# Kernel tuning notes

Hardware: AMD Instinct MI355X
Metric: run time of the kernel (lower is better)

The kernel has to match this reference:

```python
import jax, jax.numpy as jnp
import numpy as np

N0, D, H, E0 = 50000, 128, 128, 800000
N1, E1, A, B, C = 20000, 320000, 100000, 64, 10


def _gcn(x, row, col, ew, n, W, b):
    # GCNConv: out = D^-1/2 (A + I) D^-1/2 (x W) + b, with edge weights
    xw = x @ W
    sl = jnp.arange(n)
    r = jnp.concatenate([row, sl])
    c = jnp.concatenate([col, sl])
    w = jnp.concatenate([ew, jnp.ones((n,), ew.dtype)])
    deg = jax.ops.segment_sum(w, c, num_segments=n)
    dinv = jax.lax.rsqrt(jnp.maximum(deg, 1e-12))
    norm = dinv[r] * w * dinv[c]
    return jax.ops.segment_sum(norm[:, None] * xw[r], c, num_segments=n) + b


def _block(x, row, col, ew, n, W1, b1, W2, b2, Wl, bl):
    # Block with num_inner_layers=2, jumping_knowledge='cat'
    x1 = jax.nn.relu(_gcn(x, row, col, ew, n, W1, b1))
    x2 = jax.nn.relu(_gcn(x1, row, col, ew, n, W2, b2))
    return jnp.concatenate([x1, x2], axis=1) @ Wl + bl


def _seg_max(x, idx, n):
    m = jax.ops.segment_max(x, idx, num_segments=n)
    return jnp.where(jnp.isfinite(m), m, 0.0)  # empty segments -> 0 like scatter_max default


def _lin_init(k, i, o):
    s = 1.0 / np.sqrt(i)
    return jax.random.uniform(k, (i, o), jnp.float32, -s, s)


def setup_inputs() -> dict:
    key = jax.random.key(0)
    ks = jax.random.split(key, 20)
    x = jax.random.normal(ks[0], (N0, D), jnp.float32)
    edge_index0 = jax.random.randint(ks[1], (2, E0), 0, N0)
    edge_weight0 = jax.random.uniform(ks[2], (E0,), jnp.float32)
    batch0 = jnp.sort(jax.random.randint(ks[3], (N0,), 0, B))
    cover_row = jax.random.randint(ks[4], (A,), 0, N0)
    cover_col = jnp.concatenate([jnp.arange(N1), jax.random.randint(ks[5], (A - N1,), 0, N1)])
    edge_index1 = jax.random.randint(ks[6], (2, E1), 0, N1)
    edge_weight1 = jax.random.uniform(ks[7], (E1,), jnp.float32)
    batch1 = jnp.sort(jax.random.randint(ks[8], (N1,), 0, B))
    params = dict(
        w_in1=_lin_init(ks[9], D, H), b_in1=jnp.zeros((H,), jnp.float32),
        w_in2=_lin_init(ks[10], H, H), b_in2=jnp.zeros((H,), jnp.float32),
        w_in_lin=_lin_init(ks[11], 2 * H, H), b_in_lin=jnp.zeros((H,), jnp.float32),
        w_b1=_lin_init(ks[12], 2 * H, H), b_b1=jnp.zeros((H,), jnp.float32),
        w_b2=_lin_init(ks[13], H, H), b_b2=jnp.zeros((H,), jnp.float32),
        w_b_lin=_lin_init(ks[14], 2 * H, H), b_b_lin=jnp.zeros((H,), jnp.float32),
        bn_gamma=jnp.ones((4 * H,), jnp.float32), bn_beta=jnp.zeros((4 * H,), jnp.float32),
        w_l1=_lin_init(ks[15], 4 * H, H), b_l1=jnp.zeros((H,), jnp.float32),
        w_l2=_lin_init(ks[16], H, C), b_l2=jnp.zeros((C,), jnp.float32),
    )
    return dict(x=x, edge_index0=edge_index0, edge_weight0=edge_weight0, batch0=batch0,
                cover_row=cover_row, cover_col=cover_col, edge_index1=edge_index1,
                edge_weight1=edge_weight1, batch1=batch1, **params)


def reference(x, edge_index0, edge_weight0, batch0, cover_row, cover_col,
              edge_index1, edge_weight1, batch1,
              w_in1, b_in1, w_in2, b_in2, w_in_lin, b_in_lin,
              w_b1, b_b1, w_b2, b_b2, w_b_lin, b_b_lin,
              bn_gamma, bn_beta, w_l1, b_l1, w_l2, b_l2):
    r0, c0 = edge_index0[0], edge_index0[1]
    h = jax.nn.relu(_block(x, r0, c0, edge_weight0, N0, w_in1, b_in1, w_in2, b_in2, w_in_lin, b_in_lin))
    xs = [jax.ops.segment_sum(h, batch0, num_segments=B), _seg_max(h, batch0, B)]
    # cover_pool_node: add + max over k-plex cover assignments
    hg = h[cover_row]
    h2 = jnp.concatenate([jax.ops.segment_sum(hg, cover_col, num_segments=N1),
                          _seg_max(hg, cover_col, N1)], axis=1)
    r1, c1 = edge_index1[0], edge_index1[1]
    h2 = jax.nn.relu(_block(h2, r1, c1, edge_weight1, N1, w_b1, b_b1, w_b2, b_b2, w_b_lin, b_b_lin))
    xs.append(jax.ops.segment_sum(h2, batch1, num_segments=B))
    xs.append(_seg_max(h2, batch1, B))
    z = jnp.concatenate(xs, axis=1)  # [B, 4H]
    # BatchNorm1d in eval mode: running stats (mean=0, var=1), eps=1e-5
    z = z * (bn_gamma * jax.lax.rsqrt(jnp.asarray(1.0 + 1e-5, z.dtype))) + bn_beta
    z = jax.nn.relu(z @ w_l1 + b_l1)
    logits = z @ w_l2 + b_l2  # dropout skipped (eval mode)
    return jax.nn.softmax(logits, axis=-1)
```

## Files before the change

kernel.cpp:

```cpp
#include <hip/hip_runtime.h>
#include <cmath>

#define HF 128

namespace {

typedef __attribute__((ext_vector_type(8))) short short8;
typedef __attribute__((ext_vector_type(4))) float f32x4;

inline int cdiv(int a, int b) { return (a + b - 1) / b; }

__device__ inline unsigned short f2bf(float x) {
    unsigned u = __float_as_uint(x);
    return (unsigned short)((u + 0x7fffu + ((u >> 16) & 1u)) >> 16);
}
__device__ inline float bf2f(unsigned short u) {
    return __uint_as_float((unsigned)u << 16);
}
__device__ inline float bflo(unsigned v) { return __uint_as_float(v << 16); }
__device__ inline float bfhi(unsigned v) { return __uint_as_float(v & 0xffff0000u); }

#define FIXS 4194304.0f
#define FIXINV 2.384185791015625e-07f
#define SUMMASK ((1ULL << 40) - 1)

template <int K, bool AF32>
__device__ __forceinline__ void gemm_dev(int bid, const void* __restrict__ A1v, int lda1,
                                         const void* __restrict__ A2v, int lda2,
                                         const unsigned short* __restrict__ wpk,
                                         const float* __restrict__ bias, int relu,
                                         unsigned short* __restrict__ out, int N) {
    const int t = threadIdx.x;
    const int wv = t >> 6, lane = t & 63;
    const int l15 = lane & 15, lhi = lane >> 4;
    const int rbase = bid * 128 + wv * 32;

    f32x4 acc[2][8];
#pragma unroll
    for (int i = 0; i < 2; ++i)
#pragma unroll
        for (int g = 0; g < 8; ++g) acc[i][g] = {0.f, 0.f, 0.f, 0.f};

    int r[2];
#pragma unroll
    for (int ri = 0; ri < 2; ++ri) {
        int rr = rbase + ri * 16 + l15;
        r[ri] = (rr < N) ? rr : (N - 1);
    }

    for (int kc = 0; kc < K / 32; ++kc) {
        int kb = kc * 32 + lhi * 8;
        short8 a[2];
#pragma unroll
        for (int ri = 0; ri < 2; ++ri) {
            if (AF32) {
                const float* A = (const float*)A1v;
                const float* p = A + (size_t)r[ri] * lda1 + kb;
                float4 f0 = *reinterpret_cast<const float4*>(p);
                float4 f1 = *reinterpret_cast<const float4*>(p + 4);
                a[ri][0] = (short)f2bf(f0.x); a[ri][1] = (short)f2bf(f0.y);
                a[ri][2] = (short)f2bf(f0.z); a[ri][3] = (short)f2bf(f0.w);
                a[ri][4] = (short)f2bf(f1.x); a[ri][5] = (short)f2bf(f1.y);
                a[ri][6] = (short)f2bf(f1.z); a[ri][7] = (short)f2bf(f1.w);
            } else {
                const unsigned short* base;
                int kk, ld;
                if (K == 256 && kb >= 128) { base = (const unsigned short*)A2v; kk = kb - 128; ld = lda2; }
                else                       { base = (const unsigned short*)A1v; kk = kb;       ld = lda1; }
                a[ri] = *reinterpret_cast<const short8*>(base + (size_t)r[ri] * ld + kk);
            }
        }
        const unsigned short* wb = wpk + (size_t)(kc * 8) * 512 + lane * 8;
#pragma unroll
        for (int g = 0; g < 8; ++g) {
            short8 b = *reinterpret_cast<const short8*>(wb + (size_t)g * 512);
            acc[0][g] = __builtin_amdgcn_mfma_f32_16x16x32_bf16(a[0], b, acc[0][g], 0, 0, 0);
            acc[1][g] = __builtin_amdgcn_mfma_f32_16x16x32_bf16(a[1], b, acc[1][g], 0, 0, 0);
        }
    }

#pragma unroll
    for (int ri = 0; ri < 2; ++ri) {
#pragma unroll
        for (int g = 0; g < 8; ++g) {
            int col = l15 + g * 16;
            float bb = bias ? bias[col] : 0.f;
#pragma unroll
            for (int e = 0; e < 4; ++e) {
                int rr = rbase + ri * 16 + lhi * 4 + e;
                if (rr < N) {
                    float v = acc[ri][g][e] + bb;
                    if (relu) v = fmaxf(v, 0.f);
                    out[(size_t)rr * 128 + col] = f2bf(v);
                }
            }
        }
    }
}

template <int K, bool AF32>
__global__ void k_mfma_gemm(const void* __restrict__ A1v, int lda1,
                            const void* __restrict__ A2v, int lda2,
                            const unsigned short* __restrict__ wpk,
                            const float* __restrict__ bias, int relu,
                            unsigned short* __restrict__ out, int N) {
    gemm_dev<K, AF32>(blockIdx.x, A1v, lda1, A2v, lda2, wpk, bias, relu, out, N);
}

__global__ void k_prep0(const float* __restrict__ w0, const float* __restrict__ w1,
                        const float* __restrict__ w2, const float* __restrict__ w3,
                        const float* __restrict__ w4, const float* __restrict__ w5,
                        unsigned short* __restrict__ wpk,
                        const int* __restrict__ b0, int n0, const int* __restrict__ b1,
                        int n1, int B, int* __restrict__ bst0, int* __restrict__ bst1) {
    int b = blockIdx.x, t = threadIdx.x;
    if (b < 576) {
        int idx = b * 256 + t;
        const float* src; int local;
        if      (idx < 16384)  { src = w0; local = idx; }
        else if (idx < 32768)  { src = w1; local = idx - 16384; }
        else if (idx < 65536)  { src = w2; local = idx - 32768; }
        else if (idx < 98304)  { src = w3; local = idx - 65536; }
        else if (idx < 114688) { src = w4; local = idx - 98304; }
        else                   { src = w5; local = idx - 114688; }
        int e = local & 7, lane = (local >> 3) & 63, g = (local >> 9) & 7, kc = local >> 12;
        int colw = (lane & 15) + 16 * g;
        int k = kc * 32 + ((lane >> 4) << 3) + e;
        wpk[idx] = f2bf(src[k * 128 + colw]);
        return;
    }
    {
        int idx = t;
        if (idx < 2 * (B + 1)) {
            int which = idx > B;
            int bb = which ? idx - (B + 1) : idx;
            const int* arr = which ? b1 : b0;
            int lo = 0, hi = which ? n1 : n0;
            while (lo < hi) {
                int mid = (lo + hi) >> 1;
                if (arr[mid] < bb) lo = mid + 1; else hi = mid;
            }
            (which ? bst1 : bst0)[bb] = lo;
        }
    }
}

__global__ void k_prep1(const float* __restrict__ x, const unsigned short* __restrict__ wpk,
                        unsigned short* __restrict__ xw, int N0gemm, int nbG,
                        const int* __restrict__ col0, const float* __restrict__ ew0,
                        unsigned long long* __restrict__ dc0, unsigned* __restrict__ rank0,
                        int E0, int nb0,
                        const int* __restrict__ col1, const float* __restrict__ ew1,
                        unsigned long long* __restrict__ dc1, unsigned* __restrict__ rank1,
                        int E1, int nb1,
                        const int* __restrict__ ccol, int* __restrict__ ccnt,
                        unsigned* __restrict__ rankc, int A) {
    int b = blockIdx.x, t = threadIdx.x;
    if (b < nbG) {
        gemm_dev<128, true>(b, x, 128, nullptr, 0, wpk, nullptr, 0, xw, N0gemm);
        return;
    }
    b -= nbG;
    if (b < nb0) {
        int e = b * 256 + t;
        if (e < E0) {
            unsigned long long v = (1ULL << 40) | (unsigned long long)(ew0[e] * FIXS + 0.5f);
            unsigned long long old = atomicAdd(&dc0[col0[e]], v);
            rank0[e] = (unsigned)(old >> 40);
        }
        return;
    }
    b -= nb0;
    if (b < nb1) {
        int e = b * 256 + t;
        if (e < E1) {
            unsigned long long v = (1ULL << 40) | (unsigned long long)(ew1[e] * FIXS + 0.5f);
            unsigned long long old = atomicAdd(&dc1[col1[e]], v);
            rank1[e] = (unsigned)(old >> 40);
        }
        return;
    }
    b -= nb1;
    {
        int e = b * 256 + t;
        if (e < A) rankc[e] = (unsigned)atomicAdd(&ccnt[ccol[e]], 1);
    }
}

__device__ inline void scan256(int* s, int v, int gid, int n, int* __restrict__ excl,
                               int* __restrict__ partial, int pb) {
    s[threadIdx.x] = v;
    __syncthreads();
    for (int off = 1; off < 256; off <<= 1) {
        int t = (threadIdx.x >= off) ? s[threadIdx.x - off] : 0;
        __syncthreads();
        s[threadIdx.x] += t;
        __syncthreads();
    }
    if (gid < n) excl[gid] = s[threadIdx.x] - v;
    if (threadIdx.x == 255) partial[pb] = s[255];
}

__global__ void k_scan_dinv(const unsigned long long* __restrict__ dc0, int* __restrict__ rp0,
                            int* __restrict__ part0, int n0, int nbs0,
                            const unsigned long long* __restrict__ dc1, int* __restrict__ rp1,
                            int* __restrict__ part1, int n1, int nbs1,
                            const int* __restrict__ ccnt, int* __restrict__ crp,
                            int* __restrict__ cpart, int nc, int nbsc,
                            float* __restrict__ dinv0, float* __restrict__ dinv1,
                            int nbd0, int nbd1) {
    __shared__ int s[256];
    int b = blockIdx.x, t = threadIdx.x;
    if (b < nbs0) {
        int gid = b * 256 + t;
        int v = (gid < n0) ? (int)(dc0[gid] >> 40) : 0;
        scan256(s, v, gid, n0, rp0, part0, b);
        return;
    }
    b -= nbs0;
    if (b < nbs1) {
        int gid = b * 256 + t;
        int v = (gid < n1) ? (int)(dc1[gid] >> 40) : 0;
        scan256(s, v, gid, n1, rp1, part1, b);
        return;
    }
    b -= nbs1;
    if (b < nbsc) {
        int gid = b * 256 + t;
        int v = (gid < nc) ? ccnt[gid] : 0;
        scan256(s, v, gid, nc, crp, cpart, b);
        return;
    }
    b -= nbsc;
    if (b < nbd0) {
        int i = b * 256 + t;
        if (i < n0) dinv0[i] = rsqrtf(1.0f + (float)(dc0[i] & SUMMASK) * FIXINV);
        return;
    }
    b -= nbd0;
    {
        int i = b * 256 + t;
        if (i < n1) dinv1[i] = rsqrtf(1.0f + (float)(dc1[i] & SUMMASK) * FIXINV);
    }
}

__global__ void k_scan2x3(int* __restrict__ p0, int nb0, int* __restrict__ p1, int nb1,
                          int* __restrict__ p2, int nb2) {
    __shared__ int s[256];
    int* p; int nb;
    if (blockIdx.x == 0)      { p = p0; nb = nb0; }
    else if (blockIdx.x == 1) { p = p1; nb = nb1; }
    else                      { p = p2; nb = nb2; }
    int v = (threadIdx.x < nb) ? p[threadIdx.x] : 0;
    s[threadIdx.x] = v;
    __syncthreads();
    for (int off = 1; off < 256; off <<= 1) {
        int t = (threadIdx.x >= off) ? s[threadIdx.x - off] : 0;
        __syncthreads();
        s[threadIdx.x] += t;
        __syncthreads();
    }
    if (threadIdx.x < nb) p[threadIdx.x] = s[threadIdx.x] - v;
}

__global__ void k_scan3x3(int* __restrict__ rp0, const int* __restrict__ part0,
                          int n0, int tot0, int nb0,
                          int* __restrict__ rp1, const int* __restrict__ part1,
                          int n1, int tot1, int nb1,
                          int* __restrict__ crp, const int* __restrict__ cpart,
                          int nc, int totc) {
    int b = blockIdx.x, t = threadIdx.x;
    if (b < nb0) {
        int gid = b * 256 + t;
        if (gid < n0) rp0[gid] += part0[b];
        if (gid == 0) rp0[n0] = tot0;
        return;
    }
    b -= nb0;
    if (b < nb1) {
        int gid = b * 256 + t;
        if (gid < n1) rp1[gid] += part1[b];
        if (gid == 0) rp1[n1] = tot1;
        return;
    }
    b -= nb1;
    {
        int gid = b * 256 + t;
        if (gid < nc) crp[gid] += cpart[b];
        if (gid == 0) crp[nc] = totc;
    }
}

#define EPB 2048
__global__ void k_fillx3(const int* __restrict__ row0, const int* __restrict__ col0,
                         const float* __restrict__ ew0, const unsigned* __restrict__ rank0,
                         const float* __restrict__ dinv0, const int* __restrict__ rp0,
                         int2* __restrict__ ed0, int E0, int N0n, int g0b,
                         const int* __restrict__ row1, const int* __restrict__ col1,
                         const float* __restrict__ ew1, const unsigned* __restrict__ rank1,
                         const float* __restrict__ dinv1, const int* __restrict__ rp1,
                         int2* __restrict__ ed1, int E1, int N1n, int g1b,
                         const int* __restrict__ crow, const int* __restrict__ ccol,
                         const unsigned* __restrict__ rankc, const int* __restrict__ crp,
                         int* __restrict__ csrcs, int A) {
    int b = blockIdx.x, t = threadIdx.x;
    if (b < g0b) {
        int xcd = b & 7, chunk = b >> 3;
        int lo = (int)((long long)N0n * xcd >> 3), hi = (int)((long long)N0n * (xcd + 1) >> 3);
        int base = chunk * EPB;
#pragma unroll
        for (int i = 0; i < EPB; i += 256) {
            int e = base + i + t;
            if (e < E0) {
                int c = col0[e];
                if (c >= lo && c < hi) {
                    int r = row0[e];
                    ed0[rp0[c] + rank0[e]] =
                        make_int2(r, __float_as_int(ew0[e] * dinv0[r] * dinv0[c]));
                }
            }
        }
        return;
    }
    b -= g0b;
    if (b < g1b) {
        int xcd = b & 7, chunk = b >> 3;
        int lo = (int)((long long)N1n * xcd >> 3), hi = (int)((long long)N1n * (xcd + 1) >> 3);
        int base = chunk * EPB;
#pragma unroll
        for (int i = 0; i < EPB; i += 256) {
            int e = base + i + t;
            if (e < E1) {
                int c = col1[e];
                if (c >= lo && c < hi) {
                    int r = row1[e];
                    ed1[rp1[c] + rank1[e]] =
                        make_int2(r, __float_as_int(ew1[e] * dinv1[r] * dinv1[c]));
                }
            }
        }
        return;
    }
    b -= g1b;
    {
        int xcd = b & 7, chunk = b >> 3;
        int lo = (int)((long long)N1n * xcd >> 3), hi = (int)((long long)N1n * (xcd + 1) >> 3);
        int base = chunk * EPB;
#pragma unroll
        for (int i = 0; i < EPB; i += 256) {
            int e = base + i + t;
            if (e < A) {
                int c = ccol[e];
                if (c >= lo && c < hi) csrcs[crp[c] + rankc[e]] = crow[e];
            }
        }
    }
}

__global__ void k_gcn_gather(const unsigned* __restrict__ xw, const int* __restrict__ rowptr,
                             const int2* __restrict__ ed, const float* __restrict__ dinv,
                             const float* __restrict__ bias, unsigned* __restrict__ out, int n) {
    int wid = (blockIdx.x * 256 + threadIdx.x) >> 6;
    if (wid >= n) return;
    int lane = threadIdx.x & 63;
    int s = rowptr[wid], e = rowptr[wid + 1];
    float d = dinv[wid];
    unsigned v = xw[(size_t)wid * 64 + lane];
    float ax = bflo(v) * d * d, ay = bfhi(v) * d * d;
    float bx = 0.f, by = 0.f, cx = 0.f, cy = 0.f, dx = 0.f, dy = 0.f;
    int i = s;
    if ((i & 1) && i < e) {
        int2 e0 = ed[i];
        unsigned v0 = xw[(size_t)e0.x * 64 + lane];
        float c0 = __int_as_float(e0.y);
        ax += c0 * bflo(v0); ay += c0 * bfhi(v0);
        ++i;
    }
    for (; i + 4 <= e; i += 4) {
        int4 q0 = *reinterpret_cast<const int4*>(ed + i);
        int4 q1 = *reinterpret_cast<const int4*>(ed + i + 2);
        unsigned v0 = xw[(size_t)q0.x * 64 + lane];
        unsigned v1 = xw[(size_t)q0.z * 64 + lane];
        unsigned v2 = xw[(size_t)q1.x * 64 + lane];
        unsigned v3 = xw[(size_t)q1.z * 64 + lane];
        float c0 = __int_as_float(q0.y), c1 = __int_as_float(q0.w);
        float c2 = __int_as_float(q1.y), c3 = __int_as_float(q1.w);
        ax += c0 * bflo(v0); ay += c0 * bfhi(v0);
        bx += c1 * bflo(v1); by += c1 * bfhi(v1);
        cx += c2 * bflo(v2); cy += c2 * bfhi(v2);
        dx += c3 * bflo(v3); dy += c3 * bfhi(v3);
    }
    for (; i < e; ++i) {
        int2 e0 = ed[i];
        unsigned v0 = xw[(size_t)e0.x * 64 + lane];
        float c0 = __int_as_float(e0.y);
        ax += c0 * bflo(v0); ay += c0 * bfhi(v0);
    }
    ax += bx + cx + dx;
    ay += by + cy + dy;
    float2 bb = *reinterpret_cast<const float2*>(bias + lane * 2);
    ax = fmaxf(ax + bb.x, 0.f);
    ay = fmaxf(ay + bb.y, 0.f);
    out[(size_t)wid * 64 + lane] = (unsigned)f2bf(ax) | ((unsigned)f2bf(ay) << 16);
}

__global__ void k_pool_cover(const unsigned short* __restrict__ h, const int* __restrict__ bst,
                             float* __restrict__ psum, float* __restrict__ pmax, int nsplit,
                             int nbpool, const unsigned* __restrict__ h32,
                             const int* __restrict__ crp, const int* __restrict__ csrcs,
                             unsigned* __restrict__ h2, int n1) {
    int t = threadIdx.x;
    if ((int)blockIdx.x < nbpool) {
        int blk = blockIdx.x;
        int b = blk / nsplit, sub = (blk % nsplit) * 2 + (t >> 7);
        int col = t & 127;
        int r0 = bst[b], r1 = bst[b + 1];
        float sum = 0.f, mx = 0.f;
        for (int r = r0 + sub; r < r1; r += 2 * nsplit) {
            float v = bf2f(h[(size_t)r * HF + col]);
            sum += v;
            mx = fmaxf(mx, v);
        }
        atomicAdd(&psum[b * HF + col], sum);
        atomicMax(reinterpret_cast<int*>(&pmax[b * HF + col]), __float_as_int(mx));
        return;
    }
    int wid = (((int)blockIdx.x - nbpool) * 256 + t) >> 6;
    if (wid >= n1) return;
    int lane = t & 63;
    int s = crp[wid], e = crp[wid + 1];
    float sx = 0.f, sy = 0.f, mx = 0.f, my = 0.f;
    for (int i = s; i < e; ++i) {
        unsigned v = h32[(size_t)csrcs[i] * 64 + lane];
        float vx = bflo(v), vy = bfhi(v);
        sx += vx; sy += vy;
        mx = fmaxf(mx, vx); my = fmaxf(my, vy);
    }
    h2[(size_t)wid * 128 + lane]      = (unsigned)f2bf(sx) | ((unsigned)f2bf(sy) << 16);
    h2[(size_t)wid * 128 + 64 + lane] = (unsigned)f2bf(mx) | ((unsigned)f2bf(my) << 16);
}

__global__ void k_pool256(const unsigned short* __restrict__ h, const int* __restrict__ bst,
                          float* __restrict__ psum, float* __restrict__ pmax, int nsplit) {
    int t = threadIdx.x;
    int blk = blockIdx.x;
    int b = blk / nsplit, sub = (blk % nsplit) * 2 + (t >> 7);
    int col = t & 127;
    int r0 = bst[b], r1 = bst[b + 1];
    float sum = 0.f, mx = 0.f;
    for (int r = r0 + sub; r < r1; r += 2 * nsplit) {
        float v = bf2f(h[(size_t)r * HF + col]);
        sum += v;
        mx = fmaxf(mx, v);
    }
    atomicAdd(&psum[b * HF + col], sum);
    atomicMax(reinterpret_cast<int*>(&pmax[b * HF + col]), __float_as_int(mx));
}

__global__ void k_head(const float* __restrict__ p0s, const float* __restrict__ p0m,
                       const float* __restrict__ p1s, const float* __restrict__ p1m,
                       const float* __restrict__ gamma, const float* __restrict__ beta,
                       const float* __restrict__ w1, const float* __restrict__ b1,
                       const float* __restrict__ w2, const float* __restrict__ b2,
                       float* __restrict__ out) {
    __shared__ float z[512];
    __shared__ float z1[128];
    __shared__ float lg[10];
    int b = blockIdx.x, t = threadIdx.x;
    const float s = rsqrtf(1.0f + 1e-5f);
    z[t]       = p0s[b * 128 + t] * (gamma[t] * s)       + beta[t];
    z[128 + t] = p0m[b * 128 + t] * (gamma[128 + t] * s) + beta[128 + t];
    z[256 + t] = p1s[b * 128 + t] * (gamma[256 + t] * s) + beta[256 + t];
    z[384 + t] = p1m[b * 128 + t] * (gamma[384 + t] * s) + beta[384 + t];
    __syncthreads();
    float acc = b1[t];
    for (int k = 0; k < 512; ++k) acc += z[k] * w1[k * 128 + t];
    z1[t] = fmaxf(acc, 0.f);
    __syncthreads();
    if (t < 10) {
        float a2 = b2[t];
        for (int k = 0; k < 128; ++k) a2 += z1[k] * w2[k * 10 + t];
        lg[t] = a2;
    }
    __syncthreads();
    if (t == 0) {
        float m = lg[0];
        for (int c = 1; c < 10; ++c) m = fmaxf(m, lg[c]);
        float e[10], ssum = 0.f;
        for (int c = 0; c < 10; ++c) { e[c] = expf(lg[c] - m); ssum += e[c]; }
        for (int c = 0; c < 10; ++c) out[b * 10 + c] = e[c] / ssum;
    }
}

}

extern "C" void kernel_launch(void* const* d_in, const int* in_sizes, int n_in,
                              void* d_out, int out_size, void* d_ws, size_t ws_size,
                              hipStream_t stream) {
    const float* x      = (const float*)d_in[0];
    const int*   ei0    = (const int*)d_in[1];
    const float* ew0    = (const float*)d_in[2];
    const int*   batch0 = (const int*)d_in[3];
    const int*   crow   = (const int*)d_in[4];
    const int*   ccol   = (const int*)d_in[5];
    const int*   ei1    = (const int*)d_in[6];
    const float* ew1    = (const float*)d_in[7];
    const int*   batch1 = (const int*)d_in[8];
    const float* w_in1  = (const float*)d_in[9];
    const float* b_in1  = (const float*)d_in[10];
    const float* w_in2  = (const float*)d_in[11];
    const float* b_in2  = (const float*)d_in[12];
    const float* w_inl  = (const float*)d_in[13];
    const float* b_inl  = (const float*)d_in[14];
    const float* w_b1   = (const float*)d_in[15];
    const float* b_b1   = (const float*)d_in[16];
    const float* w_b2   = (const float*)d_in[17];
    const float* b_b2   = (const float*)d_in[18];
    const float* w_bl   = (const float*)d_in[19];
    const float* b_bl   = (const float*)d_in[20];
    const float* gamma  = (const float*)d_in[21];
    const float* beta   = (const float*)d_in[22];
    const float* w_l1   = (const float*)d_in[23];
    const float* b_l1   = (const float*)d_in[24];
    const float* w_l2   = (const float*)d_in[25];
    const float* b_l2   = (const float*)d_in[26];

    const int N0 = in_sizes[0] / 128;
    const int E0 = in_sizes[2];
    const int A  = in_sizes[4];
    const int E1 = in_sizes[7];
    const int N1 = in_sizes[8];
    const int B  = out_size / 10;

    const int* row0 = ei0;
    const int* col0 = ei0 + E0;
    const int* row1 = ei1;
    const int* col1 = ei1 + E1;

    char* wsp = (char*)d_ws;
    size_t off = 0;
    auto alloc = [&](size_t bytes) -> char* {
        char* p = wsp + off;
        off += (bytes + 255) & ~(size_t)255;
        return p;
    };
    unsigned long long* dc0 = (unsigned long long*)alloc((size_t)N0 * 8);
    unsigned long long* dc1 = (unsigned long long*)alloc((size_t)N1 * 8);
    int*   ccnt  = (int*)alloc((size_t)N1 * 4);
    float* p0s   = (float*)alloc((size_t)B * HF * 4 * 4);
    float* p0m   = p0s + (size_t)B * HF;
    float* p1s   = p0m + (size_t)B * HF;
    float* p1m   = p1s + (size_t)B * HF;
    size_t zero_bytes = off;

    unsigned* xw  = (unsigned*)alloc((size_t)N0 * 64 * 4);
    unsigned* x1  = (unsigned*)alloc((size_t)N0 * 64 * 4);
    unsigned* x2  = (unsigned*)alloc((size_t)N0 * 64 * 4);
    unsigned* h   = (unsigned*)alloc((size_t)N0 * 64 * 4);
    unsigned* h2  = (unsigned*)alloc((size_t)N1 * 128 * 4);
    unsigned short* wpk = (unsigned short*)alloc(147456 * 2);
    float* dinv0 = (float*)alloc((size_t)N0 * 4);
    float* dinv1 = (float*)alloc((size_t)N1 * 4);
    int*   rp0   = (int*)alloc(((size_t)N0 + 1) * 4);
    int*   rp1   = (int*)alloc(((size_t)N1 + 1) * 4);
    int*   crp   = (int*)alloc(((size_t)N1 + 1) * 4);
    int*   part0 = (int*)alloc(256 * 4);
    int*   part1 = (int*)alloc(256 * 4);
    int*   cpart = (int*)alloc(256 * 4);
    int2*  ed0   = (int2*)alloc((size_t)E0 * 8);
    int2*  ed1   = (int2*)alloc((size_t)E1 * 8);
    int*   csrcs = (int*)alloc((size_t)A * 4);
    unsigned* rank0 = (unsigned*)alloc((size_t)E0 * 4);
    unsigned* rank1 = (unsigned*)alloc((size_t)E1 * 4);
    unsigned* rankc = (unsigned*)alloc((size_t)A * 4);
    int*   bst0  = (int*)alloc((size_t)(B + 1) * 4);
    int*   bst1  = (int*)alloc((size_t)(B + 1) * 4);
    (void)ws_size; (void)n_in;

    const int NSPLIT = 16;
    const int nbG  = cdiv(N0, 128);
    const int nbE0 = cdiv(E0, 256), nbE1 = cdiv(E1, 256), nbC = cdiv(A, 256);
    const int nbs0 = cdiv(N0, 256), nbs1 = cdiv(N1, 256), nbsc = cdiv(N1, 256);
    const int g0b = cdiv(E0, EPB) * 8, g1b = cdiv(E1, EPB) * 8, gcb = cdiv(A, EPB) * 8;

    hipMemsetAsync(dc0, 0, zero_bytes, stream);

    k_prep0<<<577, 256, 0, stream>>>(w_in1, w_in2, w_inl, w_b1, w_b2, w_bl, wpk,
                                     batch0, N0, batch1, N1, B, bst0, bst1);

    k_prep1<<<nbG + nbE0 + nbE1 + nbC, 256, 0, stream>>>(
        x, wpk, (unsigned short*)xw, N0, nbG,
        col0, ew0, dc0, rank0, E0, nbE0,
        col1, ew1, dc1, rank1, E1, nbE1,
        ccol, ccnt, rankc, A);

    k_scan_dinv<<<nbs0 + nbs1 + nbsc + nbs0 + nbs1, 256, 0, stream>>>(
        dc0, rp0, part0, N0, nbs0, dc1, rp1, part1, N1, nbs1,
        ccnt, crp, cpart, N1, nbsc, dinv0, dinv1, nbs0, nbs1);

    k_scan2x3<<<3, 256, 0, stream>>>(part0, nbs0, part1, nbs1, cpart, nbsc);

    k_scan3x3<<<nbs0 + nbs1 + nbsc, 256, 0, stream>>>(
        rp0, part0, N0, E0, nbs0, rp1, part1, N1, E1, nbs1, crp, cpart, N1, A);

    k_fillx3<<<g0b + g1b + gcb, 256, 0, stream>>>(
        row0, col0, ew0, rank0, dinv0, rp0, ed0, E0, N0, g0b,
        row1, col1, ew1, rank1, dinv1, rp1, ed1, E1, N1, g1b,
        crow, ccol, rankc, crp, csrcs, A);

    k_gcn_gather<<<cdiv(N0, 4), 256, 0, stream>>>(xw, rp0, ed0, dinv0, b_in1, x1, N0);
    k_mfma_gemm<128, false><<<cdiv(N0, 128), 256, 0, stream>>>(
        x1, 128, nullptr, 0, wpk + 16384, nullptr, 0, (unsigned short*)xw, N0);
    k_gcn_gather<<<cdiv(N0, 4), 256, 0, stream>>>(xw, rp0, ed0, dinv0, b_in2, x2, N0);
    k_mfma_gemm<256, false><<<cdiv(N0, 128), 256, 0, stream>>>(
        x1, 128, x2, 128, wpk + 32768, b_inl, 1, (unsigned short*)h, N0);

    k_pool_cover<<<B * NSPLIT + cdiv(N1, 4), 256, 0, stream>>>(
        (const unsigned short*)h, bst0, p0s, p0m, NSPLIT, B * NSPLIT,
        h, crp, csrcs, h2, N1);

    k_mfma_gemm<256, false><<<cdiv(N1, 128), 256, 0, stream>>>(
        h2, 256, (const unsigned short*)h2 + 128, 256, wpk + 65536, nullptr, 0,
        (unsigned short*)xw, N1);
    k_gcn_gather<<<cdiv(N1, 4), 256, 0, stream>>>(xw, rp1, ed1, dinv1, b_b1, x1, N1);
    k_mfma_gemm<128, false><<<cdiv(N1, 128), 256, 0, stream>>>(
        x1, 128, nullptr, 0, wpk + 98304, nullptr, 0, (unsigned short*)xw, N1);
    k_gcn_gather<<<cdiv(N1, 4), 256, 0, stream>>>(xw, rp1, ed1, dinv1, b_b2, x2, N1);
    k_mfma_gemm<256, false><<<cdiv(N1, 128), 256, 0, stream>>>(
        x1, 128, x2, 128, wpk + 114688, b_bl, 1, (unsigned short*)h, N1);

    k_pool256<<<B * NSPLIT, 256, 0, stream>>>((const unsigned short*)h, bst1, p1s, p1m, NSPLIT);

    k_head<<<B, 128, 0, stream>>>(p0s, p0m, p1s, p1m, gamma, beta, w_l1, b_l1, w_l2, b_l2,
                                  (float*)d_out);
}
```

Baseline: 381.1 us.

## Shard XW into column planes for gathers and overlap graph-1 preprocessing with block-0 work

GEMMs that feed GCN aggregation now write XW as four 32-column planes. The gather kernel gives each node a 16-lane quarter-wave that works on one plane, which is meant to shrink the gather working set per pass and improve L2 locality for random row reads. The graph-1 histogram, scans and CSR fill are pulled off the critical path and fused as extra blocks into the block-0 gather and GEMM launches, so they overlap with that work. This adds more kernel launches for the graph-0 scan chain, and the gather is less unrolled (two edges per iteration instead of four).

```diff
diff --git a/kernel.cpp b/kernel.cpp
--- a/kernel.cpp
+++ b/kernel.cpp
@@ -2,6 +2,7 @@
 #include <cmath>
 
 #define HF 128
+#define EPB 2048
 
 namespace {
 
@@ -24,7 +25,7 @@
 #define FIXINV 2.384185791015625e-07f
 #define SUMMASK ((1ULL << 40) - 1)
 
-template <int K, bool AF32>
+template <int K, bool AF32, bool PLANES>
 __device__ __forceinline__ void gemm_dev(int bid, const void* __restrict__ A1v, int lda1,
                                          const void* __restrict__ A2v, int lda2,
                                          const unsigned short* __restrict__ wpk,
@@ -91,20 +92,110 @@
                 if (rr < N) {
                     float v = acc[ri][g][e] + bb;
                     if (relu) v = fmaxf(v, 0.f);
-                    out[(size_t)rr * 128 + col] = f2bf(v);
+                    if (PLANES)
+                        out[(size_t)(col >> 5) * ((size_t)N * 32) + (size_t)rr * 32 + (col & 31)] = f2bf(v);
+                    else
+                        out[(size_t)rr * 128 + col] = f2bf(v);
                 }
             }
         }
     }
 }
 
-template <int K, bool AF32>
+template <int K, bool AF32, bool PLANES>
 __global__ void k_mfma_gemm(const void* __restrict__ A1v, int lda1,
                             const void* __restrict__ A2v, int lda2,
                             const unsigned short* __restrict__ wpk,
                             const float* __restrict__ bias, int relu,
                             unsigned short* __restrict__ out, int N) {
-    gemm_dev<K, AF32>(blockIdx.x, A1v, lda1, A2v, lda2, wpk, bias, relu, out, N);
+    gemm_dev<K, AF32, PLANES>(blockIdx.x, A1v, lda1, A2v, lda2, wpk, bias, relu, out, N);
+}
+
+__device__ __forceinline__ void hist_dev(int e, int E, const int* __restrict__ col,
+                                         const float* __restrict__ ew,
+                                         unsigned long long* __restrict__ dc,
+                                         unsigned* __restrict__ rank) {
+    if (e < E) {
+        unsigned long long v = (1ULL << 40) | (unsigned long long)(ew[e] * FIXS + 0.5f);
+        unsigned long long old = atomicAdd(&dc[col[e]], v);
+        rank[e] = (unsigned)(old >> 40);
+    }
+}
+
+__device__ inline void scan256(int* s, int v, int gid, int n, int* __restrict__ excl,
+                               int* __restrict__ partial, int pb) {
+    s[threadIdx.x] = v;
+    __syncthreads();
+    for (int off = 1; off < 256; off <<= 1) {
+        int t = (threadIdx.x >= off) ? s[threadIdx.x - off] : 0;
+        __syncthreads();
+        s[threadIdx.x] += t;
+        __syncthreads();
+    }
+    if (gid < n) excl[gid] = s[threadIdx.x] - v;
+    if (threadIdx.x == 255) partial[pb] = s[255];
+}
+
+__device__ __forceinline__ void fill_dev(int b, int t, const int* __restrict__ row,
+                                         const int* __restrict__ col, const float* __restrict__ ew,
+                                         const unsigned* __restrict__ rank,
+                                         const float* __restrict__ dinv, const int* __restrict__ rp,
+                                         int2* __restrict__ ed, int E, int Nn) {
+    int xcd = b & 7, chunk = b >> 3;
+    int lo = (int)((long long)Nn * xcd >> 3), hi = (int)((long long)Nn * (xcd + 1) >> 3);
+    int base = chunk * EPB;
+#pragma unroll
+    for (int i = 0; i < EPB; i += 256) {
+        int e = base + i + t;
+        if (e < E) {
+            int c = col[e];
+            if (c >= lo && c < hi) {
+                int r = row[e];
+                ed[rp[c] + rank[e]] = make_int2(r, __float_as_int(ew[e] * dinv[r] * dinv[c]));
+            }
+        }
+    }
+}
+
+__device__ __forceinline__ void gather_dev(int b, const unsigned* __restrict__ xwp, int n,
+                                           const int* __restrict__ rp, const int2* __restrict__ ed,
+                                           const float* __restrict__ dinv,
+                                           const float* __restrict__ bias,
+                                           unsigned* __restrict__ out) {
+    int t = threadIdx.x;
+    int shard = b & 3;
+    int lane = t & 63, wv = t >> 6;
+    int dl = lane >> 4, l16 = lane & 15;
+    int wid = (b >> 2) * 16 + wv * 4 + dl;
+    if (wid >= n) return;
+    const unsigned* plane = xwp + (size_t)shard * ((size_t)n * 16);
+    int s = rp[wid], e = rp[wid + 1];
+    float d = dinv[wid];
+    unsigned v = plane[(size_t)wid * 16 + l16];
+    float ax = bflo(v) * d * d, ay = bfhi(v) * d * d, bx = 0.f, by = 0.f;
+    int i = s;
+    for (; i + 2 <= e; i += 2) {
+        unsigned long long p0 = __builtin_nontemporal_load((const unsigned long long*)(ed + i));
+        unsigned long long p1 = __builtin_nontemporal_load((const unsigned long long*)(ed + i + 1));
+        unsigned v0 = plane[(size_t)(unsigned)(p0 & 0xffffffffu) * 16 + l16];
+        unsigned v1 = plane[(size_t)(unsigned)(p1 & 0xffffffffu) * 16 + l16];
+        float c0 = __uint_as_float((unsigned)(p0 >> 32));
+        float c1 = __uint_as_float((unsigned)(p1 >> 32));
+        ax += c0 * bflo(v0); ay += c0 * bfhi(v0);
+        bx += c1 * bflo(v1); by += c1 * bfhi(v1);
+    }
+    if (i < e) {
+        int2 e0 = ed[i];
+        unsigned v0 = plane[(size_t)e0.x * 16 + l16];
+        float c0 = __int_as_float(e0.y);
+        ax += c0 * bflo(v0); ay += c0 * bfhi(v0);
+    }
+    ax += bx; ay += by;
+    float2 bb = *reinterpret_cast<const float2*>(bias + shard * 32 + l16 * 2);
+    ax = fmaxf(ax + bb.x, 0.f);
+    ay = fmaxf(ay + bb.y, 0.f);
+    unsigned o = (unsigned)f2bf(ax) | ((unsigned)f2bf(ay) << 16);
+    __builtin_nontemporal_store(o, out + (size_t)wid * 64 + shard * 16 + l16);
 }
 
 __global__ void k_prep0(const float* __restrict__ w0, const float* __restrict__ w1,
@@ -129,19 +220,17 @@
         wpk[idx] = f2bf(src[k * 128 + colw]);
         return;
     }
-    {
-        int idx = t;
-        if (idx < 2 * (B + 1)) {
-            int which = idx > B;
-            int bb = which ? idx - (B + 1) : idx;
-            const int* arr = which ? b1 : b0;
-            int lo = 0, hi = which ? n1 : n0;
-            while (lo < hi) {
-                int mid = (lo + hi) >> 1;
-                if (arr[mid] < bb) lo = mid + 1; else hi = mid;
-            }
-            (which ? bst1 : bst0)[bb] = lo;
+    int idx = t;
+    if (idx < 2 * (B + 1)) {
+        int which = idx > B;
+        int bb = which ? idx - (B + 1) : idx;
+        const int* arr = which ? b1 : b0;
+        int lo = 0, hi = which ? n1 : n0;
+        while (lo < hi) {
+            int mid = (lo + hi) >> 1;
+            if (arr[mid] < bb) lo = mid + 1; else hi = mid;
         }
+        (which ? bst1 : bst0)[bb] = lo;
     }
 }
 
@@ -149,46 +238,28 @@
                         unsigned short* __restrict__ xw, int N0gemm, int nbG,
                         const int* __restrict__ col0, const float* __restrict__ ew0,
                         unsigned long long* __restrict__ dc0, unsigned* __restrict__ rank0,
-                        int E0, int nb0,
-                        const int* __restrict__ col1, const float* __restrict__ ew1,
-                        unsigned long long* __restrict__ dc1, unsigned* __restrict__ rank1,
-                        int E1, int nb1,
-                        const int* __restrict__ ccol, int* __restrict__ ccnt,
-                        unsigned* __restrict__ rankc, int A) {
-    int b = blockIdx.x, t = threadIdx.x;
+                        int E0) {
+    int b = blockIdx.x;
     if (b < nbG) {
-        gemm_dev<128, true>(b, x, 128, nullptr, 0, wpk, nullptr, 0, xw, N0gemm);
+        gemm_dev<128, true, true>(b, x, 128, nullptr, 0, wpk, nullptr, 0, xw, N0gemm);
         return;
     }
     b -= nbG;
-    if (b < nb0) {
-        int e = b * 256 + t;
-        if (e < E0) {
-            unsigned long long v = (1ULL << 40) | (unsigned long long)(ew0[e] * FIXS + 0.5f);
-            unsigned long long old = atomicAdd(&dc0[col0[e]], v);
-            rank0[e] = (unsigned)(old >> 40);
-        }
-        return;
-    }
-    b -= nb0;
-    if (b < nb1) {
-        int e = b * 256 + t;
-        if (e < E1) {
-            unsigned long long v = (1ULL << 40) | (unsigned long long)(ew1[e] * FIXS + 0.5f);
-            unsigned long long old = atomicAdd(&dc1[col1[e]], v);
-            rank1[e] = (unsigned)(old >> 40);
-        }
-        return;
-    }
-    b -= nb1;
-    {
-        int e = b * 256 + t;
-        if (e < A) rankc[e] = (unsigned)atomicAdd(&ccnt[ccol[e]], 1);
-    }
-}
-
-__device__ inline void scan256(int* s, int v, int gid, int n, int* __restrict__ excl,
-                               int* __restrict__ partial, int pb) {
+    hist_dev(b * 256 + (int)threadIdx.x, E0, col0, ew0, dc0, rank0);
+}
+
+__global__ void k_scanA(const unsigned long long* __restrict__ dc0, int* __restrict__ rp0,
+                        int* __restrict__ part0, float* __restrict__ dinv0, int n0) {
+    __shared__ int s[256];
+    int gid = blockIdx.x * 256 + threadIdx.x;
+    int v = (gid < n0) ? (int)(dc0[gid] >> 40) : 0;
+    scan256(s, v, gid, n0, rp0, part0, blockIdx.x);
+    if (gid < n0) dinv0[gid] = rsqrtf(1.0f + (float)(dc0[gid] & SUMMASK) * FIXINV);
+}
+
+__global__ void k_scan2a(int* __restrict__ p0, int nb0) {
+    __shared__ int s[256];
+    int v = (threadIdx.x < nb0) ? p0[threadIdx.x] : 0;
     s[threadIdx.x] = v;
     __syncthreads();
     for (int off = 1; off < 256; off <<= 1) {
@@ -197,60 +268,73 @@
         s[threadIdx.x] += t;
         __syncthreads();
     }
-    if (gid < n) excl[gid] = s[threadIdx.x] - v;
-    if (threadIdx.x == 255) partial[pb] = s[255];
-}
-
-__global__ void k_scan_dinv(const unsigned long long* __restrict__ dc0, int* __restrict__ rp0,
-                            int* __restrict__ part0, int n0, int nbs0,
+    if (threadIdx.x < nb0) p0[threadIdx.x] = s[threadIdx.x] - v;
+}
+
+__global__ void k_scan3a(int* __restrict__ rp0, const int* __restrict__ part0, int n0, int tot) {
+    int gid = blockIdx.x * 256 + threadIdx.x;
+    if (gid < n0) rp0[gid] += part0[blockIdx.x];
+    if (gid == 0) rp0[n0] = tot;
+}
+
+__global__ void k_fill0(const int* __restrict__ row0, const int* __restrict__ col0,
+                        const float* __restrict__ ew0, const unsigned* __restrict__ rank0,
+                        const float* __restrict__ dinv0, const int* __restrict__ rp0,
+                        int2* __restrict__ ed0, int E0, int N0n) {
+    fill_dev(blockIdx.x, threadIdx.x, row0, col0, ew0, rank0, dinv0, rp0, ed0, E0, N0n);
+}
+
+__global__ void k_gather_hist(const unsigned* __restrict__ xwp, int n,
+                              const int* __restrict__ rp, const int2* __restrict__ ed,
+                              const float* __restrict__ dinv, const float* __restrict__ bias,
+                              unsigned* __restrict__ out, int G,
+                              const int* __restrict__ col1, const float* __restrict__ ew1,
+                              unsigned long long* __restrict__ dc1, unsigned* __restrict__ rank1,
+                              int E1, int nb1,
+                              const int* __restrict__ ccol, int* __restrict__ ccnt,
+                              unsigned* __restrict__ rankc, int A) {
+    int b = blockIdx.x;
+    if (b < G) { gather_dev(b, xwp, n, rp, ed, dinv, bias, out); return; }
+    b -= G;
+    int t = threadIdx.x;
+    if (b < nb1) { hist_dev(b * 256 + t, E1, col1, ew1, dc1, rank1); return; }
+    b -= nb1;
+    int e = b * 256 + t;
+    if (e < A) rankc[e] = (unsigned)atomicAdd(&ccnt[ccol[e]], 1);
+}
+
+__global__ void k_gemm_scan(const void* __restrict__ A1v, const unsigned short* __restrict__ wpk,
+                            unsigned short* __restrict__ out, int N, int nbG,
                             const unsigned long long* __restrict__ dc1, int* __restrict__ rp1,
-                            int* __restrict__ part1, int n1, int nbs1,
+                            int* __restrict__ part1, float* __restrict__ dinv1, int n1, int nbs1,
                             const int* __restrict__ ccnt, int* __restrict__ crp,
-                            int* __restrict__ cpart, int nc, int nbsc,
-                            float* __restrict__ dinv0, float* __restrict__ dinv1,
-                            int nbd0, int nbd1) {
+                            int* __restrict__ cpart, int nc) {
     __shared__ int s[256];
-    int b = blockIdx.x, t = threadIdx.x;
-    if (b < nbs0) {
-        int gid = b * 256 + t;
-        int v = (gid < n0) ? (int)(dc0[gid] >> 40) : 0;
-        scan256(s, v, gid, n0, rp0, part0, b);
+    int b = blockIdx.x;
+    if (b < nbG) {
+        gemm_dev<128, false, true>(b, A1v, 128, nullptr, 0, wpk, nullptr, 0, out, N);
         return;
     }
-    b -= nbs0;
+    b -= nbG;
     if (b < nbs1) {
-        int gid = b * 256 + t;
+        int gid = b * 256 + threadIdx.x;
         int v = (gid < n1) ? (int)(dc1[gid] >> 40) : 0;
         scan256(s, v, gid, n1, rp1, part1, b);
+        if (gid < n1) dinv1[gid] = rsqrtf(1.0f + (float)(dc1[gid] & SUMMASK) * FIXINV);
         return;
     }
     b -= nbs1;
-    if (b < nbsc) {
-        int gid = b * 256 + t;
+    {
+        int gid = b * 256 + threadIdx.x;
         int v = (gid < nc) ? ccnt[gid] : 0;
         scan256(s, v, gid, nc, crp, cpart, b);
-        return;
-    }
-    b -= nbsc;
-    if (b < nbd0) {
-        int i = b * 256 + t;
-        if (i < n0) dinv0[i] = rsqrtf(1.0f + (float)(dc0[i] & SUMMASK) * FIXINV);
-        return;
-    }
-    b -= nbd0;
-    {
-        int i = b * 256 + t;
-        if (i < n1) dinv1[i] = rsqrtf(1.0f + (float)(dc1[i] & SUMMASK) * FIXINV);
-    }
-}
-
-__global__ void k_scan2x3(int* __restrict__ p0, int nb0, int* __restrict__ p1, int nb1,
-                          int* __restrict__ p2, int nb2) {
+    }
+}
+
+__global__ void k_scan2b(int* __restrict__ p1, int nb1, int* __restrict__ p2, int nb2) {
     __shared__ int s[256];
-    int* p; int nb;
-    if (blockIdx.x == 0)      { p = p0; nb = nb0; }
-    else if (blockIdx.x == 1) { p = p1; nb = nb1; }
-    else                      { p = p2; nb = nb2; }
+    int* p = (blockIdx.x == 0) ? p1 : p2;
+    int nb = (blockIdx.x == 0) ? nb1 : nb2;
     int v = (threadIdx.x < nb) ? p[threadIdx.x] : 0;
     s[threadIdx.x] = v;
     __syncthreads();
@@ -263,20 +347,10 @@
     if (threadIdx.x < nb) p[threadIdx.x] = s[threadIdx.x] - v;
 }
 
-__global__ void k_scan3x3(int* __restrict__ rp0, const int* __restrict__ part0,
-                          int n0, int tot0, int nb0,
-                          int* __restrict__ rp1, const int* __restrict__ part1,
-                          int n1, int tot1, int nb1,
-                          int* __restrict__ crp, const int* __restrict__ cpart,
-                          int nc, int totc) {
+__global__ void k_scan3b(int* __restrict__ rp1, const int* __restrict__ part1, int n1, int tot1,
+                         int nb1, int* __restrict__ crp, const int* __restrict__ cpart,
+                         int nc, int totc) {
     int b = blockIdx.x, t = threadIdx.x;
-    if (b < nb0) {
-        int gid = b * 256 + t;
-        if (gid < n0) rp0[gid] += part0[b];
-        if (gid == 0) rp0[n0] = tot0;
-        return;
-    }
-    b -= nb0;
     if (b < nb1) {
         int gid = b * 256 + t;
         if (gid < n1) rp1[gid] += part1[b];
@@ -284,63 +358,26 @@
         return;
     }
     b -= nb1;
-    {
-        int gid = b * 256 + t;
-        if (gid < nc) crp[gid] += cpart[b];
-        if (gid == 0) crp[nc] = totc;
-    }
-}
-
-#define EPB 2048
-__global__ void k_fillx3(const int* __restrict__ row0, const int* __restrict__ col0,
-                         const float* __restrict__ ew0, const unsigned* __restrict__ rank0,
-                         const float* __restrict__ dinv0, const int* __restrict__ rp0,
-                         int2* __restrict__ ed0, int E0, int N0n, int g0b,
-                         const int* __restrict__ row1, const int* __restrict__ col1,
-                         const float* __restrict__ ew1, const unsigned* __restrict__ rank1,
-                         const float* __restrict__ dinv1, const int* __restrict__ rp1,
-                         int2* __restrict__ ed1, int E1, int N1n, int g1b,
-                         const int* __restrict__ crow, const int* __restrict__ ccol,
-                         const unsigned* __restrict__ rankc, const int* __restrict__ crp,
-                         int* __restrict__ csrcs, int A) {
+    int gid = b * 256 + t;
+    if (gid < nc) crp[gid] += cpart[b];
+    if (gid == 0) crp[nc] = totc;
+}
+
+__global__ void k_gather_fill(const unsigned* __restrict__ xwp, int n,
+                              const int* __restrict__ rp, const int2* __restrict__ ed,
+                              const float* __restrict__ dinv, const float* __restrict__ bias,
+                              unsigned* __restrict__ out, int G,
+                              const int* __restrict__ row1, const int* __restrict__ col1,
+                              const float* __restrict__ ew1, const unsigned* __restrict__ rank1,
+                              const float* __restrict__ dinv1, const int* __restrict__ rp1,
+                              int2* __restrict__ ed1, int E1, int N1n, int g1b,
+                              const int* __restrict__ crow, const int* __restrict__ ccol,
+                              const unsigned* __restrict__ rankc, const int* __restrict__ crp,
+                              int* __restrict__ csrcs, int A) {
     int b = blockIdx.x, t = threadIdx.x;
-    if (b < g0b) {
-        int xcd = b & 7, chunk = b >> 3;
-        int lo = (int)((long long)N0n * xcd >> 3), hi = (int)((long long)N0n * (xcd + 1) >> 3);
-        int base = chunk * EPB;
-#pragma unroll
-        for (int i = 0; i < EPB; i += 256) {
-            int e = base + i + t;
-            if (e < E0) {
-                int c = col0[e];
-                if (c >= lo && c < hi) {
-                    int r = row0[e];
-                    ed0[rp0[c] + rank0[e]] =
-                        make_int2(r, __float_as_int(ew0[e] * dinv0[r] * dinv0[c]));
-                }
-            }
-        }
-        return;
-    }
-    b -= g0b;
-    if (b < g1b) {
-        int xcd = b & 7, chunk = b >> 3;
-        int lo = (int)((long long)N1n * xcd >> 3), hi = (int)((long long)N1n * (xcd + 1) >> 3);
-        int base = chunk * EPB;
-#pragma unroll
-        for (int i = 0; i < EPB; i += 256) {
-            int e = base + i + t;
-            if (e < E1) {
-                int c = col1[e];
-                if (c >= lo && c < hi) {
-                    int r = row1[e];
-                    ed1[rp1[c] + rank1[e]] =
-                        make_int2(r, __float_as_int(ew1[e] * dinv1[r] * dinv1[c]));
-                }
-            }
-        }
-        return;
-    }
+    if (b < G) { gather_dev(b, xwp, n, rp, ed, dinv, bias, out); return; }
+    b -= G;
+    if (b < g1b) { fill_dev(b, t, row1, col1, ew1, rank1, dinv1, rp1, ed1, E1, N1n); return; }
     b -= g1b;
     {
         int xcd = b & 7, chunk = b >> 3;
@@ -357,51 +394,10 @@
     }
 }
 
-__global__ void k_gcn_gather(const unsigned* __restrict__ xw, const int* __restrict__ rowptr,
-                             const int2* __restrict__ ed, const float* __restrict__ dinv,
-                             const float* __restrict__ bias, unsigned* __restrict__ out, int n) {
-    int wid = (blockIdx.x * 256 + threadIdx.x) >> 6;
-    if (wid >= n) return;
-    int lane = threadIdx.x & 63;
-    int s = rowptr[wid], e = rowptr[wid + 1];
-    float d = dinv[wid];
-    unsigned v = xw[(size_t)wid * 64 + lane];
-    float ax = bflo(v) * d * d, ay = bfhi(v) * d * d;
-    float bx = 0.f, by = 0.f, cx = 0.f, cy = 0.f, dx = 0.f, dy = 0.f;
-    int i = s;
-    if ((i & 1) && i < e) {
-        int2 e0 = ed[i];
-        unsigned v0 = xw[(size_t)e0.x * 64 + lane];
-        float c0 = __int_as_float(e0.y);
-        ax += c0 * bflo(v0); ay += c0 * bfhi(v0);
-        ++i;
-    }
-    for (; i + 4 <= e; i += 4) {
-        int4 q0 = *reinterpret_cast<const int4*>(ed + i);
-        int4 q1 = *reinterpret_cast<const int4*>(ed + i + 2);
-        unsigned v0 = xw[(size_t)q0.x * 64 + lane];
-        unsigned v1 = xw[(size_t)q0.z * 64 + lane];
-        unsigned v2 = xw[(size_t)q1.x * 64 + lane];
-        unsigned v3 = xw[(size_t)q1.z * 64 + lane];
-        float c0 = __int_as_float(q0.y), c1 = __int_as_float(q0.w);
-        float c2 = __int_as_float(q1.y), c3 = __int_as_float(q1.w);
-        ax += c0 * bflo(v0); ay += c0 * bfhi(v0);
-        bx += c1 * bflo(v1); by += c1 * bfhi(v1);
-        cx += c2 * bflo(v2); cy += c2 * bfhi(v2);
-        dx += c3 * bflo(v3); dy += c3 * bfhi(v3);
-    }
-    for (; i < e; ++i) {
-        int2 e0 = ed[i];
-        unsigned v0 = xw[(size_t)e0.x * 64 + lane];
-        float c0 = __int_as_float(e0.y);
-        ax += c0 * bflo(v0); ay += c0 * bfhi(v0);
-    }
-    ax += bx + cx + dx;
-    ay += by + cy + dy;
-    float2 bb = *reinterpret_cast<const float2*>(bias + lane * 2);
-    ax = fmaxf(ax + bb.x, 0.f);
-    ay = fmaxf(ay + bb.y, 0.f);
-    out[(size_t)wid * 64 + lane] = (unsigned)f2bf(ax) | ((unsigned)f2bf(ay) << 16);
+__global__ void k_gather(const unsigned* __restrict__ xwp, int n, const int* __restrict__ rp,
+                         const int2* __restrict__ ed, const float* __restrict__ dinv,
+                         const float* __restrict__ bias, unsigned* __restrict__ out) {
+    gather_dev(blockIdx.x, xwp, n, rp, ed, dinv, bias, out);
 }
 
 __global__ void k_pool_cover(const unsigned short* __restrict__ h, const int* __restrict__ bst,
@@ -578,56 +574,59 @@
     (void)ws_size; (void)n_in;
 
     const int NSPLIT = 16;
-    const int nbG  = cdiv(N0, 128);
+    const int nbG0 = cdiv(N0, 128), nbG1 = cdiv(N1, 128);
     const int nbE0 = cdiv(E0, 256), nbE1 = cdiv(E1, 256), nbC = cdiv(A, 256);
     const int nbs0 = cdiv(N0, 256), nbs1 = cdiv(N1, 256), nbsc = cdiv(N1, 256);
-    const int g0b = cdiv(E0, EPB) * 8, g1b = cdiv(E1, EPB) * 8, gcb = cdiv(A, EPB) * 8;
+    const int g0f = cdiv(E0, EPB) * 8, g1f = cdiv(E1, EPB) * 8, gcf = cdiv(A, EPB) * 8;
+    const int G0 = cdiv(N0, 16) * 4, G1 = cdiv(N1, 16) * 4;
 
     hipMemsetAsync(dc0, 0, zero_bytes, stream);
 
     k_prep0<<<577, 256, 0, stream>>>(w_in1, w_in2, w_inl, w_b1, w_b2, w_bl, wpk,
                                      batch0, N0, batch1, N1, B, bst0, bst1);
 
-    k_prep1<<<nbG + nbE0 + nbE1 + nbC, 256, 0, stream>>>(
-        x, wpk, (unsigned short*)xw, N0, nbG,
-        col0, ew0, dc0, rank0, E0, nbE0,
-        col1, ew1, dc1, rank1, E1, nbE1,
-        ccol, ccnt, rankc, A);
-
-    k_scan_dinv<<<nbs0 + nbs1 + nbsc + nbs0 + nbs1, 256, 0, stream>>>(
-        dc0, rp0, part0, N0, nbs0, dc1, rp1, part1, N1, nbs1,
-        ccnt, crp, cpart, N1, nbsc, dinv0, dinv1, nbs0, nbs1);
-
-    k_scan2x3<<<3, 256, 0, stream>>>(part0, nbs0, part1, nbs1, cpart, nbsc);
-
-    k_scan3x3<<<nbs0 + nbs1 + nbsc, 256, 0, stream>>>(
-        rp0, part0, N0, E0, nbs0, rp1, part1, N1, E1, nbs1, crp, cpart, N1, A);
-
-    k_fillx3<<<g0b + g1b + gcb, 256, 0, stream>>>(
-        row0, col0, ew0, rank0, dinv0, rp0, ed0, E0, N0, g0b,
-        row1, col1, ew1, rank1, dinv1, rp1, ed1, E1, N1, g1b,
+    k_prep1<<<nbG0 + nbE0, 256, 0, stream>>>(x, wpk, (unsigned short*)xw, N0, nbG0,
+                                             col0, ew0, dc0, rank0, E0);
+
+    k_scanA<<<nbs0, 256, 0, stream>>>(dc0, rp0, part0, dinv0, N0);
+    k_scan2a<<<1, 256, 0, stream>>>(part0, nbs0);
+    k_scan3a<<<nbs0, 256, 0, stream>>>(rp0, part0, N0, E0);
+    k_fill0<<<g0f, 256, 0, stream>>>(row0, col0, ew0, rank0, dinv0, rp0, ed0, E0, N0);
+
+    k_gather_hist<<<G0 + nbE1 + nbC, 256, 0, stream>>>(
+        xw, N0, rp0, ed0, dinv0, b_in1, x1, G0,
+        col1, ew1, dc1, rank1, E1, nbE1, ccol, ccnt, rankc, A);
+
+    k_gemm_scan<<<nbG0 + nbs1 + nbsc, 256, 0, stream>>>(
+        x1, wpk + 16384, (unsigned short*)xw, N0, nbG0,
+        dc1, rp1, part1, dinv1, N1, nbs1, ccnt, crp, cpart, N1);
+
+    k_scan2b<<<2, 256, 0, stream>>>(part1, nbs1, cpart, nbsc);
+    k_scan3b<<<nbs1 + nbsc, 256, 0, stream>>>(rp1, part1, N1, E1, nbs1, crp, cpart, N1, A);
+
+    k_gather_fill<<<G0 + g1f + gcf, 256, 0, stream>>>(
+        xw, N0, rp0, ed0, dinv0, b_in2, x2, G0,
+        row1, col1, ew1, rank1, dinv1, rp1, ed1, E1, N1, g1f,
         crow, ccol, rankc, crp, csrcs, A);
 
-    k_gcn_gather<<<cdiv(N0, 4), 256, 0, stream>>>(xw, rp0, ed0, dinv0, b_in1, x1, N0);
-    k_mfma_gemm<128, false><<<cdiv(N0, 128), 256, 0, stream>>>(
-        x1, 128, nullptr, 0, wpk + 16384, nullptr, 0, (unsigned short*)xw, N0);
-    k_gcn_gather<<<cdiv(N0, 4), 256, 0, stream>>>(xw, rp0, ed0, dinv0, b_in2, x2, N0);
-    k_mfma_gemm<256, false><<<cdiv(N0, 128), 256, 0, stream>>>(
-        x1, 128, x2, 128, wpk + 32768, b_inl, 1, (unsigned short*)h, N0);
+    k_mfma_gemm<256, false, false><<<nbG0, 256, 0, stream>>>(
+        x1, 128, (const unsigned short*)x2, 128, wpk + 32768, b_inl, 1,
+        (unsigned short*)h, N0);
 
     k_pool_cover<<<B * NSPLIT + cdiv(N1, 4), 256, 0, stream>>>(
         (const unsigned short*)h, bst0, p0s, p0m, NSPLIT, B * NSPLIT,
         h, crp, csrcs, h2, N1);
 
-    k_mfma_gemm<256, false><<<cdiv(N1, 128), 256, 0, stream>>>(
+    k_mfma_gemm<256, false, true><<<nbG1, 256, 0, stream>>>(
         h2, 256, (const unsigned short*)h2 + 128, 256, wpk + 65536, nullptr, 0,
         (unsigned short*)xw, N1);
-    k_gcn_gather<<<cdiv(N1, 4), 256, 0, stream>>>(xw, rp1, ed1, dinv1, b_b1, x1, N1);
-    k_mfma_gemm<128, false><<<cdiv(N1, 128), 256, 0, stream>>>(
+    k_gather<<<G1, 256, 0, stream>>>(xw, N1, rp1, ed1, dinv1, b_b1, x1);
+    k_mfma_gemm<128, false, true><<<nbG1, 256, 0, stream>>>(
         x1, 128, nullptr, 0, wpk + 98304, nullptr, 0, (unsigned short*)xw, N1);
-    k_gcn_gather<<<cdiv(N1, 4), 256, 0, stream>>>(xw, rp1, ed1, dinv1, b_b2, x2, N1);
-    k_mfma_gemm<256, false><<<cdiv(N1, 128), 256, 0, stream>>>(
-        x1, 128, x2, 128, wpk + 114688, b_bl, 1, (unsigned short*)h, N1);
+    k_gather<<<G1, 256, 0, stream>>>(xw, N1, rp1, ed1, dinv1, b_b2, x2);
+    k_mfma_gemm<256, false, false><<<nbG1, 256, 0, stream>>>(
+        x1, 128, (const unsigned short*)x2, 128, wpk + 114688, b_bl, 1,
+        (unsigned short*)h, N1);
 
     k_pool256<<<B * NSPLIT, 256, 0, stream>>>((const unsigned short*)h, bst1, p1s, p1m, NSPLIT);
 
```

After: 489.7 us. +28.5%, slower.
